# Performance work log

Hardware: AMD Instinct MI355X
Metric: run time of the kernel (lower is better)

## Reference

```python
import jax, jax.numpy as jnp
import numpy as np

TOKENS = 16384
INPUT_SIZE = 4096
NUM_EXPERTS = 64
TOP_K = 8


def setup_inputs() -> dict:
    key = jax.random.key(0)
    k1, k2 = jax.random.split(key)
    hidden_states = jax.random.normal(k1, (TOKENS, INPUT_SIZE), dtype=jnp.float32)
    # nn.Linear(input_size, num_experts, bias=False) -> weight [num_experts, input_size]
    router_weight = jax.random.normal(k2, (NUM_EXPERTS, INPUT_SIZE), dtype=jnp.float32) * (INPUT_SIZE ** -0.5)
    return {"hidden_states": hidden_states, "router_weight": router_weight}


def reference(hidden_states, router_weight):
    # logits = hidden_states @ W^T : [tokens, num_experts]
    logits = jnp.einsum('th,eh->te', hidden_states, router_weight)
    # top-k over experts; lax.top_k values == gather(logits, topk indices)
    top_k_logits, top_k_idx = jax.lax.top_k(logits, TOP_K)
    top_k_gates = jax.nn.softmax(top_k_logits.astype(jnp.float32), axis=-1)
    return top_k_idx, top_k_gates
```

## Files before the change

kernel.cpp:

```cpp
#include <hip/hip_runtime.h>
#include <math.h>

#define TOKENS 16384
#define HID    4096
#define NEXP   64
#define TOPK   8
#define BT     64
#define BK     64
#define NTILES (HID / BK)
#define TAU    5e-4f
#define REFINE_BLOCKS 1024

typedef short          bf16x8 __attribute__((ext_vector_type(8)));
typedef unsigned short u16x8  __attribute__((ext_vector_type(8)));
typedef float          f32x4  __attribute__((ext_vector_type(4)));

#define BUF_STRIDE 32768
#define AHI 0
#define ALO 8192
#define BHI 16384
#define BLO 24576

__device__ __forceinline__ unsigned short bf16_rtn(float x) {
    unsigned u = __builtin_bit_cast(unsigned, x);
    u += 0x7FFFu + ((u >> 16) & 1u);
    return (unsigned short)(u >> 16);
}

__device__ __forceinline__ void splitf(float x, unsigned short& h, unsigned short& l) {
    h = bf16_rtn(x);
    float hf = __builtin_bit_cast(float, (unsigned)h << 16);
    l = bf16_rtn(x - hf);
}

__global__ void zero_cnt_kernel(int* cnt) {
    if (threadIdx.x == 0) cnt[0] = 0;
}

__global__ __launch_bounds__(256) void moe_gate_pass1(
    const float* __restrict__ hs,
    const float* __restrict__ w,
    float* __restrict__ out_idx_f,
    float* __restrict__ out_gate,
    int* __restrict__ flag_cnt,
    int* __restrict__ flag_list,
    int flag_cap)
{
    __shared__ char lds[65536];
    const int tid = threadIdx.x;
    const int t0  = blockIdx.x * BT;

    const int arow = tid >> 2;
    const int kq   = (tid & 3) << 4;
    const size_t abase = (size_t)(t0 + arow) * HID + kq;
    const size_t bbase = (size_t)arow * HID + kq;

    const int lane = tid & 63;
    const int wv   = tid >> 6;
    const int wm   = wv & 1;
    const int wn   = wv >> 1;
    const int sw   = (lane & 7) << 4;
    const int kgb  = (lane >> 4) << 4;
    const int aoff0 = (wm * 32 + (lane & 15)) * 128 + kgb;
    const int boff0 = (wn * 32 + (lane & 15)) * 128 + kgb;

    float areg[16], breg[16];
    u16x8 vah[2], val_[2], vbh[2], vbl[2];

    f32x4 acc[2][2];
    #pragma unroll
    for (int i = 0; i < 2; ++i)
        #pragma unroll
        for (int j = 0; j < 2; ++j) {
            acc[i][j][0] = 0.f; acc[i][j][1] = 0.f;
            acc[i][j][2] = 0.f; acc[i][j][3] = 0.f;
        }

    auto LOADS = [&](int t) {
        const f32x4* pa = (const f32x4*)(hs + abase + (size_t)t * BK);
        const f32x4* pb = (const f32x4*)(w  + bbase + (size_t)t * BK);
        #pragma unroll
        for (int i = 0; i < 4; ++i) {
            ((f32x4*)areg)[i] = pa[i];
            ((f32x4*)breg)[i] = pb[i];
        }
    };

    auto CONV = [&]() {
        #pragma unroll
        for (int c = 0; c < 2; ++c)
            #pragma unroll
            for (int i = 0; i < 8; ++i) {
                unsigned short h, l;
                splitf(areg[c * 8 + i], h, l); vah[c][i] = h; val_[c][i] = l;
                splitf(breg[c * 8 + i], h, l); vbh[c][i] = h; vbl[c][i] = l;
            }
    };

    auto WRITE = [&](int buf) {
        char* bp = lds + buf * BUF_STRIDE;
        const int base = arow * 128 + (kq << 1);
        const int swz  = (arow & 7) << 4;
        *(u16x8*)(bp + AHI + ((base +  0) ^ swz)) = vah[0];
        *(u16x8*)(bp + AHI + ((base + 16) ^ swz)) = vah[1];
        *(u16x8*)(bp + ALO + ((base +  0) ^ swz)) = val_[0];
        *(u16x8*)(bp + ALO + ((base + 16) ^ swz)) = val_[1];
        *(u16x8*)(bp + BHI + ((base +  0) ^ swz)) = vbh[0];
        *(u16x8*)(bp + BHI + ((base + 16) ^ swz)) = vbh[1];
        *(u16x8*)(bp + BLO + ((base +  0) ^ swz)) = vbl[0];
        *(u16x8*)(bp + BLO + ((base + 16) ^ swz)) = vbl[1];
    };

    auto COMPUTE = [&](int buf) {
        const char* bp = lds + buf * BUF_STRIDE;
        #pragma unroll
        for (int kk = 0; kk < 2; ++kk) {
            bf16x8 fah[2], fal[2], fbh[2], fbl[2];
            #pragma unroll
            for (int mi = 0; mi < 2; ++mi) {
                int ao = (aoff0 + mi * 16 * 128 + kk * 64) ^ sw;
                fah[mi] = *(const bf16x8*)(bp + AHI + ao);
                fal[mi] = *(const bf16x8*)(bp + ALO + ao);
            }
            #pragma unroll
            for (int ni = 0; ni < 2; ++ni) {
                int bo = (boff0 + ni * 16 * 128 + kk * 64) ^ sw;
                fbh[ni] = *(const bf16x8*)(bp + BHI + bo);
                fbl[ni] = *(const bf16x8*)(bp + BLO + bo);
            }
            #pragma unroll
            for (int mi = 0; mi < 2; ++mi)
                #pragma unroll
                for (int ni = 0; ni < 2; ++ni) {
                    acc[mi][ni] = __builtin_amdgcn_mfma_f32_16x16x32_bf16(
                        fah[mi], fbh[ni], acc[mi][ni], 0, 0, 0);
                    acc[mi][ni] = __builtin_amdgcn_mfma_f32_16x16x32_bf16(
                        fah[mi], fbl[ni], acc[mi][ni], 0, 0, 0);
                    acc[mi][ni] = __builtin_amdgcn_mfma_f32_16x16x32_bf16(
                        fal[mi], fbh[ni], acc[mi][ni], 0, 0, 0);
                }
        }
    };

    LOADS(0);
    CONV();
    WRITE(0);
    __syncthreads();
    LOADS(1);
    int cur = 0;
    for (int t = 0; t < NTILES - 1; ++t) {
        COMPUTE(cur);
        CONV();
        if (t < NTILES - 2) LOADS(t + 2);
        __syncthreads();
        WRITE(cur ^ 1);
        __syncthreads();
        cur ^= 1;
    }
    COMPUTE(cur);
    __syncthreads();

    float* lg = (float*)lds;
    #pragma unroll
    for (int mi = 0; mi < 2; ++mi)
        #pragma unroll
        for (int ni = 0; ni < 2; ++ni)
            #pragma unroll
            for (int r = 0; r < 4; ++r) {
                int trow = wm * 32 + mi * 16 + ((lane >> 4) << 2) + r;
                int col  = wn * 32 + ni * 16 + (lane & 15);
                lg[trow * 65 + col] = acc[mi][ni][r];
            }
    __syncthreads();

    if (tid < BT) {
        const int t = tid;
        float v[9];
        int   id[9];
        #pragma unroll
        for (int j = 0; j < 9; ++j) { v[j] = -INFINITY; id[j] = -1; }
        for (int e = 0; e < NEXP; ++e) {
            float x = lg[t * 65 + e];
            if (x > v[8]) {
                int p = 8;
                while (p > 0 && v[p - 1] < x) {
                    v[p]  = v[p - 1];
                    id[p] = id[p - 1];
                    --p;
                }
                v[p]  = x;
                id[p] = e;
            }
        }
        float g = v[0] - v[1];
        #pragma unroll
        for (int j = 1; j < 8; ++j) g = fminf(g, v[j] - v[j + 1]);

        bool deferred = false;
        if (g < TAU) {
            int slot = atomicAdd(flag_cnt, 1);
            if (slot < flag_cap) {
                flag_list[slot] = t0 + t;
                deferred = true;
            }
        }
        if (!deferred) {
            float m = v[0];
            float ex[TOPK];
            float s = 0.0f;
            #pragma unroll
            for (int j = 0; j < TOPK; ++j) { ex[j] = expf(v[j] - m); s += ex[j]; }
            float inv = 1.0f / s;
            size_t base = (size_t)(t0 + t) * TOPK;
            #pragma unroll
            for (int j = 0; j < TOPK; ++j) {
                out_idx_f[base + j] = (float)id[j];
                out_gate[base + j]  = ex[j] * inv;
            }
        }
    }
}

__global__ __launch_bounds__(256) void moe_gate_refine(
    const float* __restrict__ hs,
    const float* __restrict__ w,
    float* __restrict__ out_idx_f,
    float* __restrict__ out_gate,
    const int* __restrict__ flag_cnt,
    const int* __restrict__ flag_list,
    int flag_cap)
{
    __shared__ float  hrow[HID];
    __shared__ double lgw[4][NEXP];
    __shared__ double lgd[NEXP];
    const int tid  = threadIdx.x;
    const int lane = tid & 63;
    const int wv   = tid >> 6;

    int n = flag_cnt[0];
    if (n > flag_cap) n = flag_cap;

    for (int fi = blockIdx.x; fi < n; fi += gridDim.x) {
        const int t = flag_list[fi];
        #pragma unroll
        for (int i = 0; i < 4; ++i)
            ((f32x4*)hrow)[tid + 256 * i] =
                ((const f32x4*)(hs + (size_t)t * HID))[tid + 256 * i];
        __syncthreads();

        for (int e = 0; e < NEXP; ++e) {
            const f32x4* wp = (const f32x4*)(w + (size_t)e * HID);
            double s0 = 0.0, s1 = 0.0, s2 = 0.0, s3 = 0.0;
            #pragma unroll
            for (int i = 0; i < 4; ++i) {
                f32x4 wf = wp[tid + 256 * i];
                f32x4 af = ((const f32x4*)hrow)[tid + 256 * i];
                s0 = fma((double)wf[0], (double)af[0], s0);
                s1 = fma((double)wf[1], (double)af[1], s1);
                s2 = fma((double)wf[2], (double)af[2], s2);
                s3 = fma((double)wf[3], (double)af[3], s3);
            }
            double d = (s0 + s1) + (s2 + s3);
            #pragma unroll
            for (int off = 32; off > 0; off >>= 1)
                d += __shfl_down(d, off, 64);
            if (lane == 0) lgw[wv][e] = d;
        }
        __syncthreads();
        if (tid < NEXP)
            lgd[tid] = (lgw[0][tid] + lgw[1][tid]) + (lgw[2][tid] + lgw[3][tid]);
        __syncthreads();

        if (tid == 0) {
            double v[TOPK];
            int    id[TOPK];
            #pragma unroll
            for (int j = 0; j < TOPK; ++j) { v[j] = -INFINITY; id[j] = -1; }
            for (int e = 0; e < NEXP; ++e) {
                double x = lgd[e];
                if (x > v[TOPK - 1]) {
                    int p = TOPK - 1;
                    while (p > 0 && v[p - 1] < x) {
                        v[p]  = v[p - 1];
                        id[p] = id[p - 1];
                        --p;
                    }
                    v[p]  = x;
                    id[p] = e;
                }
            }
            double m = v[0];
            double ex[TOPK];
            double s = 0.0;
            #pragma unroll
            for (int j = 0; j < TOPK; ++j) { ex[j] = exp(v[j] - m); s += ex[j]; }
            double inv = 1.0 / s;
            size_t base = (size_t)t * TOPK;
            #pragma unroll
            for (int j = 0; j < TOPK; ++j) {
                out_idx_f[base + j] = (float)id[j];
                out_gate[base + j]  = (float)(ex[j] * inv);
            }
        }
        __syncthreads();
    }
}

extern "C" void kernel_launch(void* const* d_in, const int* in_sizes, int n_in,
                              void* d_out, int out_size, void* d_ws, size_t ws_size,
                              hipStream_t stream) {
    const float* hs = (const float*)d_in[0];
    const float* w  = (const float*)d_in[1];
    float* out      = (float*)d_out;
    float* out_idx  = out;
    float* out_gate = out + (size_t)TOKENS * TOPK;

    int* flag_cnt  = (int*)d_ws;
    int* flag_list = flag_cnt + 1;
    int flag_cap   = (int)(ws_size / sizeof(int)) - 1;
    if (flag_cap > TOKENS) flag_cap = TOKENS;
    if (flag_cap < 0) flag_cap = 0;

    hipLaunchKernelGGL(zero_cnt_kernel, dim3(1), dim3(64), 0, stream, flag_cnt);
    hipLaunchKernelGGL(moe_gate_pass1, dim3(TOKENS / BT), dim3(256), 0, stream,
                       hs, w, out_idx, out_gate, flag_cnt, flag_list, flag_cap);
    hipLaunchKernelGGL(moe_gate_refine, dim3(REFINE_BLOCKS), dim3(256), 0, stream,
                       hs, w, out_idx, out_gate, flag_cnt, flag_list, flag_cap);
}
```

Before: 175.3 us.

## Pre-split router weights to bf16 hi/lo and use split-K register-direct GEMM

Adds a prep kernel that converts the router weight once per call into bf16 hi/lo arrays in workspace, and also zeroes the flag counter. The pass1 GEMM now handles 16 tokens per block and splits K across four waves. Operands are loaded straight from global memory into registers with a software prefetch pipeline, so the LDS staging and per-tile barriers are gone. Partial sums are reduced through LDS before top-k. This removes LDS traffic and redundant weight conversion, at the cost of more global weight reads per token (64 experts per 16 tokens) and a dependence on L2 reuse of the weights.

```diff
diff --git a/kernel.cpp b/kernel.cpp
--- a/kernel.cpp
+++ b/kernel.cpp
@@ -5,21 +5,15 @@
 #define HID    4096
 #define NEXP   64
 #define TOPK   8
-#define BT     64
-#define BK     64
-#define NTILES (HID / BK)
+#define KSPLIT 4
+#define WK     (HID / KSPLIT)
+#define NSTEP  (WK / 32)
 #define TAU    5e-4f
 #define REFINE_BLOCKS 1024
 
 typedef short          bf16x8 __attribute__((ext_vector_type(8)));
 typedef unsigned short u16x8  __attribute__((ext_vector_type(8)));
 typedef float          f32x4  __attribute__((ext_vector_type(4)));
-
-#define BUF_STRIDE 32768
-#define AHI 0
-#define ALO 8192
-#define BHI 16384
-#define BLO 24576
 
 __device__ __forceinline__ unsigned short bf16_rtn(float x) {
     unsigned u = __builtin_bit_cast(unsigned, x);
@@ -33,154 +27,117 @@
     l = bf16_rtn(x - hf);
 }
 
-__global__ void zero_cnt_kernel(int* cnt) {
-    if (threadIdx.x == 0) cnt[0] = 0;
+__global__ __launch_bounds__(256) void prep_kernel(
+    const float* __restrict__ w,
+    unsigned short* __restrict__ whi,
+    unsigned short* __restrict__ wlo,
+    int* __restrict__ flag_cnt)
+{
+    if (blockIdx.x == 0 && threadIdx.x == 0) flag_cnt[0] = 0;
+    int gid = blockIdx.x * 256 + threadIdx.x;
+    const f32x4* wp = (const f32x4*)w;
+    f32x4 v0 = wp[gid * 2 + 0];
+    f32x4 v1 = wp[gid * 2 + 1];
+    u16x8 h8, l8;
+    #pragma unroll
+    for (int j = 0; j < 8; ++j) {
+        float x = (j < 4) ? v0[j] : v1[j - 4];
+        unsigned short h, l;
+        splitf(x, h, l);
+        h8[j] = h; l8[j] = l;
+    }
+    *(u16x8*)(whi + (size_t)gid * 8) = h8;
+    *(u16x8*)(wlo + (size_t)gid * 8) = l8;
 }
 
 __global__ __launch_bounds__(256) void moe_gate_pass1(
     const float* __restrict__ hs,
-    const float* __restrict__ w,
+    const unsigned short* __restrict__ whi,
+    const unsigned short* __restrict__ wlo,
     float* __restrict__ out_idx_f,
     float* __restrict__ out_gate,
     int* __restrict__ flag_cnt,
     int* __restrict__ flag_list,
     int flag_cap)
 {
-    __shared__ char lds[65536];
-    const int tid = threadIdx.x;
-    const int t0  = blockIdx.x * BT;
-
-    const int arow = tid >> 2;
-    const int kq   = (tid & 3) << 4;
-    const size_t abase = (size_t)(t0 + arow) * HID + kq;
-    const size_t bbase = (size_t)arow * HID + kq;
-
+    __shared__ float part[KSPLIT][16][68];
+
+    const int tid  = threadIdx.x;
     const int lane = tid & 63;
     const int wv   = tid >> 6;
-    const int wm   = wv & 1;
-    const int wn   = wv >> 1;
-    const int sw   = (lane & 7) << 4;
-    const int kgb  = (lane >> 4) << 4;
-    const int aoff0 = (wm * 32 + (lane & 15)) * 128 + kgb;
-    const int boff0 = (wn * 32 + (lane & 15)) * 128 + kgb;
-
-    float areg[16], breg[16];
-    u16x8 vah[2], val_[2], vbh[2], vbl[2];
-
-    f32x4 acc[2][2];
+    const int t0   = blockIdx.x * 16;
+    const int row  = lane & 15;
+    const int kg   = (lane >> 4) * 8;
+    const size_t kbase = (size_t)wv * WK;
+
+    const float*          ap  = hs  + (size_t)(t0 + row) * HID + kbase + kg;
+    const unsigned short* bhp = whi + (size_t)row * HID + kbase + kg;
+    const unsigned short* blp = wlo + (size_t)row * HID + kbase + kg;
+
+    f32x4  acc[4];
     #pragma unroll
-    for (int i = 0; i < 2; ++i)
-        #pragma unroll
-        for (int j = 0; j < 2; ++j) {
-            acc[i][j][0] = 0.f; acc[i][j][1] = 0.f;
-            acc[i][j][2] = 0.f; acc[i][j][3] = 0.f;
-        }
-
-    auto LOADS = [&](int t) {
-        const f32x4* pa = (const f32x4*)(hs + abase + (size_t)t * BK);
-        const f32x4* pb = (const f32x4*)(w  + bbase + (size_t)t * BK);
-        #pragma unroll
-        for (int i = 0; i < 4; ++i) {
-            ((f32x4*)areg)[i] = pa[i];
-            ((f32x4*)breg)[i] = pb[i];
-        }
-    };
-
-    auto CONV = [&]() {
-        #pragma unroll
-        for (int c = 0; c < 2; ++c)
-            #pragma unroll
-            for (int i = 0; i < 8; ++i) {
-                unsigned short h, l;
-                splitf(areg[c * 8 + i], h, l); vah[c][i] = h; val_[c][i] = l;
-                splitf(breg[c * 8 + i], h, l); vbh[c][i] = h; vbl[c][i] = l;
-            }
-    };
-
-    auto WRITE = [&](int buf) {
-        char* bp = lds + buf * BUF_STRIDE;
-        const int base = arow * 128 + (kq << 1);
-        const int swz  = (arow & 7) << 4;
-        *(u16x8*)(bp + AHI + ((base +  0) ^ swz)) = vah[0];
-        *(u16x8*)(bp + AHI + ((base + 16) ^ swz)) = vah[1];
-        *(u16x8*)(bp + ALO + ((base +  0) ^ swz)) = val_[0];
-        *(u16x8*)(bp + ALO + ((base + 16) ^ swz)) = val_[1];
-        *(u16x8*)(bp + BHI + ((base +  0) ^ swz)) = vbh[0];
-        *(u16x8*)(bp + BHI + ((base + 16) ^ swz)) = vbh[1];
-        *(u16x8*)(bp + BLO + ((base +  0) ^ swz)) = vbl[0];
-        *(u16x8*)(bp + BLO + ((base + 16) ^ swz)) = vbl[1];
-    };
-
-    auto COMPUTE = [&](int buf) {
-        const char* bp = lds + buf * BUF_STRIDE;
-        #pragma unroll
-        for (int kk = 0; kk < 2; ++kk) {
-            bf16x8 fah[2], fal[2], fbh[2], fbl[2];
-            #pragma unroll
-            for (int mi = 0; mi < 2; ++mi) {
-                int ao = (aoff0 + mi * 16 * 128 + kk * 64) ^ sw;
-                fah[mi] = *(const bf16x8*)(bp + AHI + ao);
-                fal[mi] = *(const bf16x8*)(bp + ALO + ao);
-            }
-            #pragma unroll
-            for (int ni = 0; ni < 2; ++ni) {
-                int bo = (boff0 + ni * 16 * 128 + kk * 64) ^ sw;
-                fbh[ni] = *(const bf16x8*)(bp + BHI + bo);
-                fbl[ni] = *(const bf16x8*)(bp + BLO + bo);
-            }
-            #pragma unroll
-            for (int mi = 0; mi < 2; ++mi)
-                #pragma unroll
-                for (int ni = 0; ni < 2; ++ni) {
-                    acc[mi][ni] = __builtin_amdgcn_mfma_f32_16x16x32_bf16(
-                        fah[mi], fbh[ni], acc[mi][ni], 0, 0, 0);
-                    acc[mi][ni] = __builtin_amdgcn_mfma_f32_16x16x32_bf16(
-                        fah[mi], fbl[ni], acc[mi][ni], 0, 0, 0);
-                    acc[mi][ni] = __builtin_amdgcn_mfma_f32_16x16x32_bf16(
-                        fal[mi], fbh[ni], acc[mi][ni], 0, 0, 0);
-                }
-        }
-    };
-
-    LOADS(0);
-    CONV();
-    WRITE(0);
+    for (int ng = 0; ng < 4; ++ng) { acc[ng][0]=0.f; acc[ng][1]=0.f; acc[ng][2]=0.f; acc[ng][3]=0.f; }
+
+    f32x4  Aq[4][2];
+    bf16x8 Bh[2][4], Bl[2][4];
+    bf16x8 fah, fal;
+
+#define LA(s, t) { const f32x4* p = (const f32x4*)(ap + (t) * 32); \
+                   Aq[s][0] = p[0]; Aq[s][1] = p[1]; }
+#define LB(s, t) { _Pragma("unroll") for (int ng = 0; ng < 4; ++ng) { \
+                     Bh[s][ng] = *(const bf16x8*)(bhp + ng * 16 * HID + (t) * 32); \
+                     Bl[s][ng] = *(const bf16x8*)(blp + ng * 16 * HID + (t) * 32); } }
+#define CONVA(s) { _Pragma("unroll") for (int j = 0; j < 8; ++j) { \
+                     float x = (j < 4) ? Aq[s][0][j] : Aq[s][1][j - 4]; \
+                     unsigned short h, l; splitf(x, h, l); \
+                     fah[j] = (short)h; fal[j] = (short)l; } }
+#define MF(bs) { _Pragma("unroll") for (int ng = 0; ng < 4; ++ng) { \
+                   acc[ng] = __builtin_amdgcn_mfma_f32_16x16x32_bf16(fah, Bh[bs][ng], acc[ng], 0, 0, 0); \
+                   acc[ng] = __builtin_amdgcn_mfma_f32_16x16x32_bf16(fah, Bl[bs][ng], acc[ng], 0, 0, 0); \
+                   acc[ng] = __builtin_amdgcn_mfma_f32_16x16x32_bf16(fal, Bh[bs][ng], acc[ng], 0, 0, 0); } }
+
+    LA(0, 0) LA(1, 1) LA(2, 2) LA(3, 3)
+    LB(0, 0)
+
+    #pragma unroll 4
+    for (int t = 0; t < NSTEP - 4; ++t) {
+        CONVA(t & 3)
+        LA((t + 4) & 3, t + 4)
+        LB((t + 1) & 1, t + 1)
+        MF(t & 1)
+    }
+    LB(1, 29) CONVA(0) MF(0)
+    LB(0, 30) CONVA(1) MF(1)
+    LB(1, 31) CONVA(2) MF(0)
+              CONVA(3) MF(1)
+
+#undef LA
+#undef LB
+#undef CONVA
+#undef MF
+
+    #pragma unroll
+    for (int ng = 0; ng < 4; ++ng)
+        #pragma unroll
+        for (int r = 0; r < 4; ++r)
+            part[wv][(lane >> 4) * 4 + r][ng * 16 + (lane & 15)] = acc[ng][r];
     __syncthreads();
-    LOADS(1);
-    int cur = 0;
-    for (int t = 0; t < NTILES - 1; ++t) {
-        COMPUTE(cur);
-        CONV();
-        if (t < NTILES - 2) LOADS(t + 2);
-        __syncthreads();
-        WRITE(cur ^ 1);
-        __syncthreads();
-        cur ^= 1;
-    }
-    COMPUTE(cur);
+
+    for (int s = tid; s < 16 * 64; s += 256) {
+        int tt = s >> 6, e = s & 63;
+        float v = part[0][tt][e] + part[1][tt][e] + part[2][tt][e] + part[3][tt][e];
+        part[0][tt][e] = v;
+    }
     __syncthreads();
 
-    float* lg = (float*)lds;
-    #pragma unroll
-    for (int mi = 0; mi < 2; ++mi)
-        #pragma unroll
-        for (int ni = 0; ni < 2; ++ni)
-            #pragma unroll
-            for (int r = 0; r < 4; ++r) {
-                int trow = wm * 32 + mi * 16 + ((lane >> 4) << 2) + r;
-                int col  = wn * 32 + ni * 16 + (lane & 15);
-                lg[trow * 65 + col] = acc[mi][ni][r];
-            }
-    __syncthreads();
-
-    if (tid < BT) {
+    if (tid < 16) {
         const int t = tid;
         float v[9];
         int   id[9];
         #pragma unroll
         for (int j = 0; j < 9; ++j) { v[j] = -INFINITY; id[j] = -1; }
         for (int e = 0; e < NEXP; ++e) {
-            float x = lg[t * 65 + e];
+            float x = part[0][t][e];
             if (x > v[8]) {
                 int p = 8;
                 while (p > 0 && v[p - 1] < x) {
@@ -315,15 +272,17 @@
     float* out_idx  = out;
     float* out_gate = out + (size_t)TOKENS * TOPK;
 
-    int* flag_cnt  = (int*)d_ws;
+    unsigned short* whi = (unsigned short*)d_ws;
+    unsigned short* wlo = whi + (size_t)NEXP * HID;
+    int* flag_cnt  = (int*)(wlo + (size_t)NEXP * HID);
     int* flag_list = flag_cnt + 1;
-    int flag_cap   = (int)(ws_size / sizeof(int)) - 1;
-    if (flag_cap > TOKENS) flag_cap = TOKENS;
-    if (flag_cap < 0) flag_cap = 0;
-
-    hipLaunchKernelGGL(zero_cnt_kernel, dim3(1), dim3(64), 0, stream, flag_cnt);
-    hipLaunchKernelGGL(moe_gate_pass1, dim3(TOKENS / BT), dim3(256), 0, stream,
-                       hs, w, out_idx, out_gate, flag_cnt, flag_list, flag_cap);
+    long flag_cap_l = ((long)ws_size - 2L * NEXP * HID * 2 - 16) / 4;
+    int flag_cap = flag_cap_l < 0 ? 0 : (flag_cap_l > TOKENS ? TOKENS : (int)flag_cap_l);
+
+    hipLaunchKernelGGL(prep_kernel, dim3(NEXP * HID / (256 * 8)), dim3(256), 0, stream,
+                       w, whi, wlo, flag_cnt);
+    hipLaunchKernelGGL(moe_gate_pass1, dim3(TOKENS / 16), dim3(256), 0, stream,
+                       hs, whi, wlo, out_idx, out_gate, flag_cnt, flag_list, flag_cap);
     hipLaunchKernelGGL(moe_gate_refine, dim3(REFINE_BLOCKS), dim3(256), 0, stream,
                        hs, w, out_idx, out_gate, flag_cnt, flag_list, flag_cap);
 }
```

Result: slower. 249.7 us (+42.4%).
